# Kernel tuning notes

Hardware: AMD Instinct MI355X
Metric: run time of the kernel (lower is better)

## Reference

```python
import jax, jax.numpy as jnp
import numpy as np

N = 50000          # nodes
E = 800000         # edges
D_IN = 64          # env INPUT_DIM
D_H = 64           # env HIDDEN_DIM
D_OUT = 32         # env OUTPUT_DIM
A_H = 16           # action HIDDEN_DIM
NUM_ENV = 3        # env NUM_LAYERS
TAU = 1.0          # gumbel temperature (fixed, LEARN_TEMPERATURE=False)
LN_EPS = 1e-5


def setup_inputs() -> dict:
    key = jax.random.key(0)
    ks = jax.random.split(key, 24)

    def lin(k, fan_in, fan_out):
        s = 1.0 / np.sqrt(fan_in)
        kw, kb = jax.random.split(k)
        W = jax.random.uniform(kw, (fan_in, fan_out), jnp.float32, -s, s)
        b = jax.random.uniform(kb, (fan_out,), jnp.float32, -s, s)
        return W, b

    inp = {}
    inp['x'] = jax.random.normal(ks[0], (N, D_IN), jnp.float32)
    inp['edge_index'] = jax.random.randint(ks[1], (2, E), 0, N, dtype=jnp.int32)

    inp['W_enc'], inp['b_enc'] = lin(ks[2], D_IN, D_H)
    env_W, env_b = [], []
    for l in range(NUM_ENV):
        W, b = lin(ks[3 + l], 2 * D_H, D_H)
        env_W.append(W); env_b.append(b)
    inp['env_W'] = jnp.stack(env_W)   # [NUM_ENV, 2*D_H, D_H]
    inp['env_b'] = jnp.stack(env_b)   # [NUM_ENV, D_H]
    inp['W_dec'], inp['b_dec'] = lin(ks[6], D_H, D_OUT)
    inp['ln_g'] = jnp.ones((D_H,), jnp.float32)
    inp['ln_b'] = jnp.zeros((D_H,), jnp.float32)
    inp['in_W1'], inp['in_b1'] = lin(ks[7], 2 * D_H, A_H)
    inp['in_W2'], inp['in_b2'] = lin(ks[8], 2 * A_H, 2)
    inp['out_W1'], inp['out_b1'] = lin(ks[9], 2 * D_H, A_H)
    inp['out_W2'], inp['out_b2'] = lin(ks[10], 2 * A_H, 2)
    return inp


def _layernorm(x, g, b):
    mu = jnp.mean(x, axis=-1, keepdims=True)
    var = jnp.var(x, axis=-1, keepdims=True)
    return (x - mu) * jax.lax.rsqrt(var + LN_EPS) * g + b


def _conv(x, src, dst, W, b, edge_weight=None):
    # WeightedGNNConv: gather x[src] -> (optional * edge_weight) -> scatter-add at dst -> lin(concat(x, agg))
    msg = x[src]                                   # [E, d]
    if edge_weight is not None:
        msg = msg * edge_weight[:, None]
    agg = jax.ops.segment_sum(msg, dst, num_segments=N)
    return jnp.concatenate([x, agg], axis=-1) @ W + b


def _action_net(x, src, dst, W1, b1, W2, b2):
    h = jax.nn.relu(_conv(x, src, dst, W1, b1))
    return _conv(h, src, dst, W2, b2)              # [N, 2] logits


def _gumbel_hard(logits, key, tau):
    u = jax.random.uniform(key, logits.shape, logits.dtype, 1e-20, 1.0)
    g = -jnp.log(-jnp.log(u))
    y = jax.nn.softmax((logits + g) / tau, axis=-1)
    y_hard = jax.nn.one_hot(jnp.argmax(y, axis=-1), logits.shape[-1], dtype=y.dtype)
    return y + jax.lax.stop_gradient(y_hard - y)   # straight-through


def reference(x, edge_index, W_enc, b_enc, env_W, env_b, W_dec, b_dec, ln_g, ln_b,
              in_W1, in_b1, in_W2, in_b2, out_W1, out_b1, out_W2, out_b2):
    src, dst = edge_index[0], edge_index[1]        # u, v
    h = x @ W_enc + b_enc                          # encoder (dropout is identity in eval)
    noise_key = jax.random.key(1234)
    ews = []
    for l in range(NUM_ENV):
        h = _layernorm(h, ln_g, ln_b)
        in_logits = _action_net(h, src, dst, in_W1, in_b1, in_W2, in_b2)
        out_logits = _action_net(h, src, dst, out_W1, out_b1, out_W2, out_b2)
        in_p = _gumbel_hard(in_logits, jax.random.fold_in(noise_key, 2 * l), TAU)
        out_p = _gumbel_hard(out_logits, jax.random.fold_in(noise_key, 2 * l + 1), TAU)
        # create_edge_weight: keep_in_prob[v] * keep_out_prob[u]
        ew = in_p[:, 0][dst] * out_p[:, 0][src]    # [E], values in {0,1}
        ews.append(ew)
        h = _conv(h, src, dst, env_W[l], env_b[l], edge_weight=ew)
    out = h @ W_dec + b_dec
    return out, jnp.stack(ews)
```

## Files before the change

### kernel.cpp

```cpp
#include <hip/hip_runtime.h>
#include <math.h>

static constexpr int NN = 50000;
static constexpr int EE = 800000;

struct TF2 { unsigned a, b; };

__host__ __device__ __forceinline__ TF2 tf2x32(unsigned k0, unsigned k1,
                                               unsigned x0, unsigned x1) {
  unsigned k2 = k0 ^ k1 ^ 0x1BD11BDAu;
  x0 += k0; x1 += k1;
#define TFR(r) { x0 += x1; x1 = (x1 << (r)) | (x1 >> (32 - (r))); x1 ^= x0; }
  TFR(13) TFR(15) TFR(26) TFR(6)
  x0 += k1; x1 += k2 + 1u;
  TFR(17) TFR(29) TFR(16) TFR(24)
  x0 += k2; x1 += k0 + 2u;
  TFR(13) TFR(15) TFR(26) TFR(6)
  x0 += k0; x1 += k1 + 3u;
  TFR(17) TFR(29) TFR(16) TFR(24)
  x0 += k1; x1 += k2 + 4u;
  TFR(13) TFR(15) TFR(26) TFR(6)
  x0 += k2; x1 += k0 + 5u;
#undef TFR
  TF2 r; r.a = x0; r.b = x1; return r;
}

__device__ __forceinline__ float u01_bits(unsigned w) {
  float fl = __uint_as_float((w >> 9) | 0x3f800000u) - 1.0f;
  return fmaxf(1e-20f, fl + 1e-20f);
}

__device__ __forceinline__ float keep01(float l0, float l1, unsigned k0, unsigned k1, int node) {
  unsigned f0 = 2u * (unsigned)node, f1 = f0 + 1u;
  TF2 t0 = tf2x32(k0, k1, 0u, f0);
  TF2 t1 = tf2x32(k0, k1, 0u, f1);
  float g0 = -logf(-logf(u01_bits(t0.a ^ t0.b)));
  float g1 = -logf(-logf(u01_bits(t1.a ^ t1.b)));
  float z0 = l0 + g0, z1 = l1 + g1;
  float m  = fmaxf(z0, z1);
  float e0 = expf(z0 - m), e1 = expf(z1 - m);
  float s  = e0 + e1;
  float y0 = e0 / s, y1 = e1 / s;
  return (y1 > y0) ? 0.0f : 1.0f;
}

__global__ void k_count(const int* __restrict__ dst, int* __restrict__ deg, int e) {
  int i = blockIdx.x * blockDim.x + threadIdx.x;
  if (i < e) atomicAdd(&deg[dst[i]], 1);
}

__global__ void k_bsum(const int* __restrict__ deg, int* __restrict__ bsum, int n) {
  int i = blockIdx.x * 256 + threadIdx.x;
  int v = (i < n) ? deg[i] : 0;
  #pragma unroll
  for (int off = 32; off; off >>= 1) v += __shfl_xor(v, off, 64);
  __shared__ int ws[4];
  if ((threadIdx.x & 63) == 0) ws[threadIdx.x >> 6] = v;
  __syncthreads();
  if (threadIdx.x == 0) bsum[blockIdx.x] = ws[0] + ws[1] + ws[2] + ws[3];
}

__global__ void k_bscan(const int* __restrict__ bsum, int* __restrict__ bpref,
                        int nb, int* __restrict__ row_ptr, int n) {
  __shared__ int s[256];
  int t = threadIdx.x;
  int v = (t < nb) ? bsum[t] : 0;
  s[t] = v; __syncthreads();
  for (int off = 1; off < 256; off <<= 1) {
    int u = (t >= off) ? s[t - off] : 0;
    __syncthreads();
    s[t] += u;
    __syncthreads();
  }
  bpref[t] = s[t] - v;
  if (t == 0) row_ptr[n] = s[255];
}

__global__ void k_prefix(const int* __restrict__ deg, const int* __restrict__ bpref,
                         int* __restrict__ row_ptr, int* __restrict__ cursor, int n) {
  __shared__ int s[256];
  int t = threadIdx.x;
  int i = blockIdx.x * 256 + t;
  int v = (i < n) ? deg[i] : 0;
  s[t] = v; __syncthreads();
  for (int off = 1; off < 256; off <<= 1) {
    int u = (t >= off) ? s[t - off] : 0;
    __syncthreads();
    s[t] += u;
    __syncthreads();
  }
  if (i < n) {
    int ex = s[t] - v + bpref[blockIdx.x];
    row_ptr[i] = ex; cursor[i] = ex;
  }
}

__global__ void k_fill(const int* __restrict__ src, const int* __restrict__ dst,
                       int* __restrict__ cursor, int* __restrict__ col, int e) {
  int i = blockIdx.x * blockDim.x + threadIdx.x;
  if (i < e) {
    int pos = atomicAdd(&cursor[dst[i]], 1);
    col[pos] = src[i];
  }
}

__global__ void k_enc_ln(const float* __restrict__ x, const float* __restrict__ W,
                         const float* __restrict__ bias, const float* __restrict__ g,
                         const float* __restrict__ bb, float* __restrict__ hln) {
  __shared__ float Ws[64 * 64];
  for (int i = threadIdx.x; i < 64 * 64; i += 256) Ws[i] = W[i];
  __syncthreads();
  int node = blockIdx.x * 4 + (threadIdx.x >> 6);
  int j = threadIdx.x & 63;
  const float* xr = x + (size_t)node * 64;
  float s = bias[j];
  #pragma unroll
  for (int i = 0; i < 64; i++) s = fmaf(xr[i], Ws[i * 64 + j], s);
  float t = s;
  #pragma unroll
  for (int off = 32; off; off >>= 1) t += __shfl_xor(t, off, 64);
  float mu = t * (1.0f / 64.0f);
  float d = s - mu;
  float q = d * d;
  #pragma unroll
  for (int off = 32; off; off >>= 1) q += __shfl_xor(q, off, 64);
  float rs = 1.0f / sqrtf(q * (1.0f / 64.0f) + 1e-5f);
  hln[(size_t)node * 64 + j] = d * rs * g[j] + bb[j];
}

__global__ void k_projAll(const float* __restrict__ hln, const float* __restrict__ envW,
                          const float* __restrict__ envb,
                          const float* __restrict__ W1i, const float* __restrict__ W1o,
                          float* __restrict__ Htop, float* __restrict__ Pbot,
                          float* __restrict__ P1, float* __restrict__ S1, int nchunk) {
  __shared__ float Ws[128 * 64];
  __shared__ float st[256];
  int t = threadIdx.x;
  for (int i = t; i < 128 * 64; i += 256) Ws[i] = envW[i];
  int w = t >> 6, lane = t & 63;
  int h = lane >> 5, jo = lane & 31;
  const float* Wg = (jo < 16) ? W1i : W1o;
  int colw = jo & 15;
  float wr[64];
  #pragma unroll
  for (int i = 0; i < 64; i++) wr[i] = Wg[(h * 64 + i) * 16 + colw];
  float bj = envb[lane];
  for (int blk = blockIdx.x; blk < nchunk; blk += gridDim.x) {
    __syncthreads();
    st[t] = hln[(size_t)blk * 256 + t];
    __syncthreads();
    const float* sv = &st[w * 64];
    float a = bj, b = 0.f, c = 0.f;
    #pragma unroll
    for (int i = 0; i < 64; i++) {
      float hv = sv[i];
      a = fmaf(hv, Ws[i * 64 + lane], a);
      b = fmaf(hv, Ws[(64 + i) * 64 + lane], b);
      c = fmaf(hv, wr[i], c);
    }
    size_t node = (size_t)blk * 4 + w;
    Htop[node * 64 + lane] = a;
    Pbot[node * 64 + lane] = b;
    if (h == 0) S1[node * 32 + jo] = c;
    else        P1[node * 32 + jo] = c;
  }
}

__global__ void k_gatherA(const float* __restrict__ P1, const float* __restrict__ S1,
                          const int* __restrict__ row_ptr, const int* __restrict__ col,
                          const float* __restrict__ inb1, const float* __restrict__ outb1,
                          const float* __restrict__ inW2, const float* __restrict__ outW2,
                          float* __restrict__ P2S2) {
  int t = threadIdx.x;
  int w = t >> 6, lane = t & 63;
  int sub = lane >> 5, j = lane & 31;
  int node = blockIdx.x * 8 + w * 2 + sub;
  int b = row_ptr[node], e = row_ptr[node + 1];
  float s0 = 0.f, s1 = 0.f;
  for (int base = b; base < e; base += 32) {
    int idx = base + j;
    int u_l = (idx < e) ? col[idx] : 0;
    int cnt = min(32, e - base);
    int k = 0;
    for (; k + 2 <= cnt; k += 2) {
      int u0 = __shfl(u_l, k, 32), u1 = __shfl(u_l, k + 1, 32);
      s0 += P1[(size_t)u0 * 32 + j];
      s1 += P1[(size_t)u1 * 32 + j];
    }
    if (k < cnt) s0 += P1[(size_t)__shfl(u_l, k, 32) * 32 + j];
  }
  float agg = s0 + s1;
  float b1j = (j < 16) ? inb1[j] : outb1[j - 16];
  float rj = fmaxf(S1[(size_t)node * 32 + j] + agg + b1j, 0.f);
  float wa0, wa1, wb0, wb1;
  if (j < 16) {
    wa0 = inW2[j * 2 + 0];  wa1 = inW2[j * 2 + 1];
    wb0 = inW2[(16 + j) * 2 + 0];  wb1 = inW2[(16 + j) * 2 + 1];
  } else {
    int j2 = j - 16;
    wa0 = outW2[j2 * 2 + 0];  wa1 = outW2[j2 * 2 + 1];
    wb0 = outW2[(16 + j2) * 2 + 0];  wb1 = outW2[(16 + j2) * 2 + 1];
  }
  float v0 = rj * wa0, v1 = rj * wa1, v2 = rj * wb0, v3 = rj * wb1;
  #pragma unroll
  for (int off = 8; off; off >>= 1) {
    v0 += __shfl_xor(v0, off, 64);
    v1 += __shfl_xor(v1, off, 64);
    v2 += __shfl_xor(v2, off, 64);
    v3 += __shfl_xor(v3, off, 64);
  }
  float* row = P2S2 + (size_t)node * 8;
  if (j == 0)  { row[0] = v2; row[1] = v3; row[4] = v0; row[5] = v1; }
  if (j == 16) { row[2] = v2; row[3] = v3; row[6] = v0; row[7] = v1; }
}

__global__ void k_gatherB(const float* __restrict__ P2S2, const int* __restrict__ row_ptr,
                          const int* __restrict__ col,
                          const float* __restrict__ inb2, const float* __restrict__ outb2,
                          float* __restrict__ keep_in, float* __restrict__ keep_out,
                          unsigned ki0, unsigned ki1, unsigned ko0, unsigned ko1) {
  int t = threadIdx.x;
  int w = t >> 6, lane = t & 63;
  int g = lane >> 4, el = lane & 15;
  int node = blockIdx.x * 16 + w * 4 + g;
  int b = row_ptr[node], e = row_ptr[node + 1];
  float a0 = 0.f, a1 = 0.f, a2 = 0.f, a3 = 0.f;
  for (int base = b; base < e; base += 16) {
    int idx = base + el;
    if (idx < e) {
      int u = col[idx];
      float4 p = *(const float4*)(P2S2 + (size_t)u * 8);
      a0 += p.x; a1 += p.y; a2 += p.z; a3 += p.w;
    }
  }
  #pragma unroll
  for (int off = 8; off; off >>= 1) {
    a0 += __shfl_xor(a0, off, 64);
    a1 += __shfl_xor(a1, off, 64);
    a2 += __shfl_xor(a2, off, 64);
    a3 += __shfl_xor(a3, off, 64);
  }
  float4 sf = *(const float4*)(P2S2 + (size_t)node * 8 + 4);
  if (el == 0)
    keep_in[node]  = keep01(sf.x + a0 + inb2[0],  sf.y + a1 + inb2[1],  ki0, ki1, node);
  else if (el == 1)
    keep_out[node] = keep01(sf.z + a2 + outb2[0], sf.w + a3 + outb2[1], ko0, ko1, node);
}

template <bool LN>
__global__ void k_aggD(const float* __restrict__ Htop, const float* __restrict__ Pbot,
                       const int* __restrict__ row_ptr, const int* __restrict__ col,
                       const int* __restrict__ src, const int* __restrict__ dst,
                       const float* __restrict__ keep_in, const float* __restrict__ keep_out,
                       float* __restrict__ ew, const float* __restrict__ g,
                       const float* __restrict__ bb, float* __restrict__ hout) {
  int t = threadIdx.x;
  int ei = blockIdx.x * 64 + t;
  if (t < 64 && ei < EE)
    ew[ei] = keep_in[dst[ei]] * keep_out[src[ei]];

  int w = t >> 6, lane = t & 63;
  int node = blockIdx.x * 4 + w;
  float ki = keep_in[node];
  int b = row_ptr[node], e = row_ptr[node + 1];
  float s0 = 0.f, s1 = 0.f, s2 = 0.f, s3 = 0.f;
  if (ki != 0.f) {
    for (int base = b; base < e; base += 64) {
      int idx = base + lane;
      int u_l = (idx < e) ? col[idx] : 0;
      float ko_l = (idx < e) ? keep_out[u_l] : 0.f;
      int cnt = min(64, e - base);
      int k = 0;
      for (; k + 4 <= cnt; k += 4) {
        int u0 = __shfl(u_l, k, 64),     u1 = __shfl(u_l, k + 1, 64),
            u2 = __shfl(u_l, k + 2, 64), u3 = __shfl(u_l, k + 3, 64);
        float w0 = __shfl(ko_l, k, 64),     w1 = __shfl(ko_l, k + 1, 64),
              w2 = __shfl(ko_l, k + 2, 64), w3 = __shfl(ko_l, k + 3, 64);
        if (w0 != 0.f) s0 += Pbot[(size_t)u0 * 64 + lane];
        if (w1 != 0.f) s1 += Pbot[(size_t)u1 * 64 + lane];
        if (w2 != 0.f) s2 += Pbot[(size_t)u2 * 64 + lane];
        if (w3 != 0.f) s3 += Pbot[(size_t)u3 * 64 + lane];
      }
      for (; k < cnt; k++) {
        int u0 = __shfl(u_l, k, 64);
        float w0 = __shfl(ko_l, k, 64);
        if (w0 != 0.f) s0 += Pbot[(size_t)u0 * 64 + lane];
      }
    }
  }
  float acc = Htop[(size_t)node * 64 + lane] + ((s0 + s1) + (s2 + s3)) * ki;
  if (LN) {
    float tt = acc;
    #pragma unroll
    for (int off = 32; off; off >>= 1) tt += __shfl_xor(tt, off, 64);
    float mu = tt * (1.0f / 64.0f);
    float d = acc - mu;
    float q = d * d;
    #pragma unroll
    for (int off = 32; off; off >>= 1) q += __shfl_xor(q, off, 64);
    float rs = 1.0f / sqrtf(q * (1.0f / 64.0f) + 1e-5f);
    hout[(size_t)node * 64 + lane] = d * rs * g[lane] + bb[lane];
  } else {
    hout[(size_t)node * 64 + lane] = acc;
  }
}

__global__ void k_dec(const float* __restrict__ h, const float* __restrict__ W,
                      const float* __restrict__ bias, float* __restrict__ out) {
  __shared__ float Ws[64 * 32];
  int t = threadIdx.x;
  for (int i = t; i < 64 * 32; i += 256) Ws[i] = W[i];
  __syncthreads();
  int node = blockIdx.x * 8 + (t >> 5);
  int j = t & 31;
  const float* hr = h + (size_t)node * 64;
  float s = bias[j];
  #pragma unroll
  for (int i = 0; i < 64; i++) s = fmaf(hr[i], Ws[i * 32 + j], s);
  out[(size_t)node * 32 + j] = s;
}

extern "C" void kernel_launch(void* const* d_in, const int* in_sizes, int n_in,
                              void* d_out, int out_size, void* d_ws, size_t ws_size,
                              hipStream_t stream) {
  const float* x      = (const float*)d_in[0];
  const int*   ei     = (const int*)  d_in[1];
  const float* W_enc  = (const float*)d_in[2];
  const float* b_enc  = (const float*)d_in[3];
  const float* env_W  = (const float*)d_in[4];
  const float* env_b  = (const float*)d_in[5];
  const float* W_dec  = (const float*)d_in[6];
  const float* b_dec  = (const float*)d_in[7];
  const float* ln_g   = (const float*)d_in[8];
  const float* ln_b   = (const float*)d_in[9];
  const float* in_W1  = (const float*)d_in[10];
  const float* in_b1  = (const float*)d_in[11];
  const float* in_W2  = (const float*)d_in[12];
  const float* in_b2  = (const float*)d_in[13];
  const float* out_W1 = (const float*)d_in[14];
  const float* out_b1 = (const float*)d_in[15];
  const float* out_W2 = (const float*)d_in[16];
  const float* out_b2 = (const float*)d_in[17];

  const int n = NN, e = EE;
  const int* src = ei;
  const int* dst = ei + e;

  float* out_h  = (float*)d_out;
  float* out_ew = out_h + (size_t)n * 32;

  size_t off = 0;
  auto alloc = [&](size_t bytes) -> void* {
    void* p = (char*)d_ws + off;
    off += (bytes + 255) & ~(size_t)255;
    return p;
  };
  float* hlnA    = (float*)alloc((size_t)n * 64 * 4);
  float* hlnB    = (float*)alloc((size_t)n * 64 * 4);
  float* Htop    = (float*)alloc((size_t)n * 64 * 4);
  float* Pbot    = (float*)alloc((size_t)n * 64 * 4);
  float* P1      = (float*)alloc((size_t)n * 32 * 4);
  float* S1      = (float*)alloc((size_t)n * 32 * 4);
  float* P2S2    = (float*)alloc((size_t)n * 8 * 4);
  float* keep_i  = (float*)alloc((size_t)n * 4);
  float* keep_o  = (float*)alloc((size_t)n * 4);
  int*   deg     = (int*)alloc((size_t)n * 4);
  int*   row_ptr = (int*)alloc((size_t)(n + 1) * 4);
  int*   cursor  = (int*)alloc((size_t)n * 4);
  int*   bsum    = (int*)alloc(256 * 4);
  int*   bpref   = (int*)alloc(256 * 4);
  int*   colA    = (int*)alloc((size_t)e * 4);
  if (off > ws_size) return;

  const int nb = (n + 255) / 256;

  hipMemsetAsync(deg, 0, (size_t)n * 4, stream);
  k_count<<<(e + 255) / 256, 256, 0, stream>>>(dst, deg, e);
  k_bsum<<<nb, 256, 0, stream>>>(deg, bsum, n);
  k_bscan<<<1, 256, 0, stream>>>(bsum, bpref, nb, row_ptr, n);
  k_prefix<<<nb, 256, 0, stream>>>(deg, bpref, row_ptr, cursor, n);
  k_fill<<<(e + 255) / 256, 256, 0, stream>>>(src, dst, cursor, colA, e);

  const int g4  = n / 4;
  const int g8  = n / 8;
  const int g16 = n / 16;

  k_enc_ln<<<g4, 256, 0, stream>>>(x, W_enc, b_enc, ln_g, ln_b, hlnA);

  float* hln = hlnA;
  float* hln_next = hlnB;
  for (int l = 0; l < 3; l++) {
    TF2 kin  = tf2x32(0u, 1234u, 0u, (unsigned)(2 * l));
    TF2 kout = tf2x32(0u, 1234u, 0u, (unsigned)(2 * l + 1));

    k_projAll<<<1250, 256, 0, stream>>>(hln, env_W + (size_t)l * 128 * 64,
                                        env_b + (size_t)l * 64, in_W1, out_W1,
                                        Htop, Pbot, P1, S1, g4);
    k_gatherA<<<g8, 256, 0, stream>>>(P1, S1, row_ptr, colA, in_b1, out_b1,
                                      in_W2, out_W2, P2S2);
    k_gatherB<<<g16, 256, 0, stream>>>(P2S2, row_ptr, colA, in_b2, out_b2,
                                       keep_i, keep_o, kin.a, kin.b, kout.a, kout.b);
    if (l < 2) {
      k_aggD<true><<<g4, 256, 0, stream>>>(Htop, Pbot, row_ptr, colA, src, dst,
                                           keep_i, keep_o, out_ew + (size_t)l * e,
                                           ln_g, ln_b, hln_next);
    } else {
      k_aggD<false><<<g4, 256, 0, stream>>>(Htop, Pbot, row_ptr, colA, src, dst,
                                            keep_i, keep_o, out_ew + (size_t)l * e,
                                            ln_g, ln_b, hln_next);
    }
    float* tmp = hln; hln = hln_next; hln_next = tmp;
  }

  k_dec<<<g8, 256, 0, stream>>>(hln, W_dec, b_dec, out_h);
}
```

Baseline: 656.8 us.

## Vectorize neighbor gathers with float4 loads across multiple edges per wave

Rewrites the gatherA and aggD neighbor aggregation so each wave processes several edges in parallel. Each lane loads a float4 slice of a neighbor row, and the partial sums are reduced with cross-lane shuffles. This replaces the serial per-edge shuffle broadcast loop, aiming to issue more independent memory requests at once and cut per-edge instruction overhead. gatherA now uses one node per wave, so it launches twice as many blocks, and the LayerNorm reductions are restructured around the float4 layout.

```diff
diff --git a/kernel.cpp b/kernel.cpp
--- a/kernel.cpp
+++ b/kernel.cpp
@@ -3,6 +3,9 @@
 
 static constexpr int NN = 50000;
 static constexpr int EE = 800000;
+
+#define SHFL_ADD4(v, off) { v.x += __shfl_xor(v.x, off, 64); v.y += __shfl_xor(v.y, off, 64); \
+                            v.z += __shfl_xor(v.z, off, 64); v.w += __shfl_xor(v.w, off, 64); }
 
 struct TF2 { unsigned a, b; };
 
@@ -173,45 +176,47 @@
                           float* __restrict__ P2S2) {
   int t = threadIdx.x;
   int w = t >> 6, lane = t & 63;
-  int sub = lane >> 5, j = lane & 31;
-  int node = blockIdx.x * 8 + w * 2 + sub;
+  int es = lane >> 3, f4 = lane & 7;
+  int node = blockIdx.x * 4 + w;
   int b = row_ptr[node], e = row_ptr[node + 1];
-  float s0 = 0.f, s1 = 0.f;
-  for (int base = b; base < e; base += 32) {
-    int idx = base + j;
-    int u_l = (idx < e) ? col[idx] : 0;
-    int cnt = min(32, e - base);
-    int k = 0;
-    for (; k + 2 <= cnt; k += 2) {
-      int u0 = __shfl(u_l, k, 32), u1 = __shfl(u_l, k + 1, 32);
-      s0 += P1[(size_t)u0 * 32 + j];
-      s1 += P1[(size_t)u1 * 32 + j];
-    }
-    if (k < cnt) s0 += P1[(size_t)__shfl(u_l, k, 32) * 32 + j];
-  }
-  float agg = s0 + s1;
-  float b1j = (j < 16) ? inb1[j] : outb1[j - 16];
-  float rj = fmaxf(S1[(size_t)node * 32 + j] + agg + b1j, 0.f);
-  float wa0, wa1, wb0, wb1;
-  if (j < 16) {
-    wa0 = inW2[j * 2 + 0];  wa1 = inW2[j * 2 + 1];
-    wb0 = inW2[(16 + j) * 2 + 0];  wb1 = inW2[(16 + j) * 2 + 1];
-  } else {
-    int j2 = j - 16;
-    wa0 = outW2[j2 * 2 + 0];  wa1 = outW2[j2 * 2 + 1];
-    wb0 = outW2[(16 + j2) * 2 + 0];  wb1 = outW2[(16 + j2) * 2 + 1];
-  }
-  float v0 = rj * wa0, v1 = rj * wa1, v2 = rj * wb0, v3 = rj * wb1;
-  #pragma unroll
-  for (int off = 8; off; off >>= 1) {
-    v0 += __shfl_xor(v0, off, 64);
-    v1 += __shfl_xor(v1, off, 64);
-    v2 += __shfl_xor(v2, off, 64);
-    v3 += __shfl_xor(v3, off, 64);
-  }
+  float4 acc = make_float4(0.f, 0.f, 0.f, 0.f);
+  for (int base = b; base < e; base += 16) {
+    int i0 = base + es, i1 = base + 8 + es;
+    if (i0 < e) {
+      float4 v = ((const float4*)(P1 + (size_t)col[i0] * 32))[f4];
+      acc.x += v.x; acc.y += v.y; acc.z += v.z; acc.w += v.w;
+    }
+    if (i1 < e) {
+      float4 v = ((const float4*)(P1 + (size_t)col[i1] * 32))[f4];
+      acc.x += v.x; acc.y += v.y; acc.z += v.z; acc.w += v.w;
+    }
+  }
+  SHFL_ADD4(acc, 8) SHFL_ADD4(acc, 16) SHFL_ADD4(acc, 32)
+  float4 s1 = ((const float4*)(S1 + (size_t)node * 32))[f4];
+  const float* bsrc = (f4 < 4) ? inb1 : outb1;
+  const float* W2   = (f4 < 4) ? inW2 : outW2;
+  int jb = (f4 & 3) * 4;
+  float4 b4 = *(const float4*)(bsrc + jb);
+  float r0 = fmaxf(s1.x + acc.x + b4.x, 0.f);
+  float r1 = fmaxf(s1.y + acc.y + b4.y, 0.f);
+  float r2 = fmaxf(s1.z + acc.z + b4.z, 0.f);
+  float r3 = fmaxf(s1.w + acc.w + b4.w, 0.f);
+  float pa0, pa1, pb0, pb1;
+  {
+    const float* Wc = W2 + jb * 2;
+    pa0 = r0 * Wc[0] + r1 * Wc[2] + r2 * Wc[4] + r3 * Wc[6];
+    pa1 = r0 * Wc[1] + r1 * Wc[3] + r2 * Wc[5] + r3 * Wc[7];
+    const float* Wd = W2 + (16 + jb) * 2;
+    pb0 = r0 * Wd[0] + r1 * Wd[2] + r2 * Wd[4] + r3 * Wd[6];
+    pb1 = r0 * Wd[1] + r1 * Wd[3] + r2 * Wd[5] + r3 * Wd[7];
+  }
+  pa0 += __shfl_xor(pa0, 1, 64); pa0 += __shfl_xor(pa0, 2, 64);
+  pa1 += __shfl_xor(pa1, 1, 64); pa1 += __shfl_xor(pa1, 2, 64);
+  pb0 += __shfl_xor(pb0, 1, 64); pb0 += __shfl_xor(pb0, 2, 64);
+  pb1 += __shfl_xor(pb1, 1, 64); pb1 += __shfl_xor(pb1, 2, 64);
   float* row = P2S2 + (size_t)node * 8;
-  if (j == 0)  { row[0] = v2; row[1] = v3; row[4] = v0; row[5] = v1; }
-  if (j == 16) { row[2] = v2; row[3] = v3; row[6] = v0; row[7] = v1; }
+  if (lane == 0) { row[0] = pb0; row[1] = pb1; row[4] = pa0; row[5] = pa1; }
+  if (lane == 4) { row[2] = pb0; row[3] = pb1; row[6] = pa0; row[7] = pa1; }
 }
 
 __global__ void k_gatherB(const float* __restrict__ P2S2, const int* __restrict__ row_ptr,
@@ -260,48 +265,57 @@
     ew[ei] = keep_in[dst[ei]] * keep_out[src[ei]];
 
   int w = t >> 6, lane = t & 63;
+  int es = lane >> 4, f4 = lane & 15;
   int node = blockIdx.x * 4 + w;
   float ki = keep_in[node];
   int b = row_ptr[node], e = row_ptr[node + 1];
-  float s0 = 0.f, s1 = 0.f, s2 = 0.f, s3 = 0.f;
+  float4 acc = make_float4(0.f, 0.f, 0.f, 0.f);
   if (ki != 0.f) {
-    for (int base = b; base < e; base += 64) {
-      int idx = base + lane;
-      int u_l = (idx < e) ? col[idx] : 0;
-      float ko_l = (idx < e) ? keep_out[u_l] : 0.f;
-      int cnt = min(64, e - base);
-      int k = 0;
-      for (; k + 4 <= cnt; k += 4) {
-        int u0 = __shfl(u_l, k, 64),     u1 = __shfl(u_l, k + 1, 64),
-            u2 = __shfl(u_l, k + 2, 64), u3 = __shfl(u_l, k + 3, 64);
-        float w0 = __shfl(ko_l, k, 64),     w1 = __shfl(ko_l, k + 1, 64),
-              w2 = __shfl(ko_l, k + 2, 64), w3 = __shfl(ko_l, k + 3, 64);
-        if (w0 != 0.f) s0 += Pbot[(size_t)u0 * 64 + lane];
-        if (w1 != 0.f) s1 += Pbot[(size_t)u1 * 64 + lane];
-        if (w2 != 0.f) s2 += Pbot[(size_t)u2 * 64 + lane];
-        if (w3 != 0.f) s3 += Pbot[(size_t)u3 * 64 + lane];
+    for (int base = b; base < e; base += 8) {
+      int i0 = base + es, i1 = base + 4 + es;
+      int u0 = 0, u1 = 0; float ko0 = 0.f, ko1 = 0.f;
+      if (i0 < e) { u0 = col[i0]; ko0 = keep_out[u0]; }
+      if (i1 < e) { u1 = col[i1]; ko1 = keep_out[u1]; }
+      if (ko0 != 0.f) {
+        float4 v = ((const float4*)(Pbot + (size_t)u0 * 64))[f4];
+        acc.x += v.x; acc.y += v.y; acc.z += v.z; acc.w += v.w;
       }
-      for (; k < cnt; k++) {
-        int u0 = __shfl(u_l, k, 64);
-        float w0 = __shfl(ko_l, k, 64);
-        if (w0 != 0.f) s0 += Pbot[(size_t)u0 * 64 + lane];
+      if (ko1 != 0.f) {
+        float4 v = ((const float4*)(Pbot + (size_t)u1 * 64))[f4];
+        acc.x += v.x; acc.y += v.y; acc.z += v.z; acc.w += v.w;
       }
     }
   }
-  float acc = Htop[(size_t)node * 64 + lane] + ((s0 + s1) + (s2 + s3)) * ki;
+  SHFL_ADD4(acc, 16) SHFL_ADD4(acc, 32)
+  float4 hv = ((const float4*)(Htop + (size_t)node * 64))[f4];
+  float4 a;
+  a.x = fmaf(acc.x, ki, hv.x);
+  a.y = fmaf(acc.y, ki, hv.y);
+  a.z = fmaf(acc.z, ki, hv.z);
+  a.w = fmaf(acc.w, ki, hv.w);
   if (LN) {
-    float tt = acc;
-    #pragma unroll
-    for (int off = 32; off; off >>= 1) tt += __shfl_xor(tt, off, 64);
-    float mu = tt * (1.0f / 64.0f);
-    float d = acc - mu;
-    float q = d * d;
-    #pragma unroll
-    for (int off = 32; off; off >>= 1) q += __shfl_xor(q, off, 64);
+    float ps = (a.x + a.y) + (a.z + a.w);
+    ps += __shfl_xor(ps, 1, 64); ps += __shfl_xor(ps, 2, 64);
+    ps += __shfl_xor(ps, 4, 64); ps += __shfl_xor(ps, 8, 64);
+    float mu = ps * (1.0f / 64.0f);
+    float4 d; d.x = a.x - mu; d.y = a.y - mu; d.z = a.z - mu; d.w = a.w - mu;
+    float q = (d.x * d.x + d.y * d.y) + (d.z * d.z + d.w * d.w);
+    q += __shfl_xor(q, 1, 64); q += __shfl_xor(q, 2, 64);
+    q += __shfl_xor(q, 4, 64); q += __shfl_xor(q, 8, 64);
     float rs = 1.0f / sqrtf(q * (1.0f / 64.0f) + 1e-5f);
-    hout[(size_t)node * 64 + lane] = d * rs * g[lane] + bb[lane];
+    if (es == 0) {
+      float4 g4 = ((const float4*)g)[f4];
+      float4 b4 = ((const float4*)bb)[f4];
+      float4 o;
+      o.x = d.x * rs * g4.x + b4.x;
+      o.y = d.y * rs * g4.y + b4.y;
+      o.z = d.z * rs * g4.z + b4.z;
+      o.w = d.w * rs * g4.w + b4.w;
+      ((float4*)(hout + (size_t)node * 64))[f4] = o;
+    }
   } else {
-    hout[(size_t)node * 64 + lane] = acc;
+    if (es == 0)
+      ((float4*)(hout + (size_t)node * 64))[f4] = a;
   }
 }
 
@@ -396,7 +410,7 @@
     k_projAll<<<1250, 256, 0, stream>>>(hln, env_W + (size_t)l * 128 * 64,
                                         env_b + (size_t)l * 64, in_W1, out_W1,
                                         Htop, Pbot, P1, S1, g4);
-    k_gatherA<<<g8, 256, 0, stream>>>(P1, S1, row_ptr, colA, in_b1, out_b1,
+    k_gatherA<<<g4, 256, 0, stream>>>(P1, S1, row_ptr, colA, in_b1, out_b1,
                                       in_W2, out_W2, P2S2);
     k_gatherB<<<g16, 256, 0, stream>>>(P2S2, row_ptr, colA, in_b2, out_b2,
                                        keep_i, keep_o, kin.a, kin.b, kout.a, kout.b);
```

Result: no change. 659.3 us (+0.4%).
